# Performance work log

Measured on AMD Instinct MI355X. Metric: run time of the kernel, lower is better.

## Reference

```python
import jax, jax.numpy as jnp
import numpy as np

N = 50000
E = 1600000
D = 128
NUM_CLASSES = 10
SLOPE = 0.01  # torch leaky_relu default


def leaky_relu(x):
    return jnp.where(x >= 0, x, SLOPE * x)


def gcn_conv(x, src, dst, norm_out, norm_in, W, b):
    # DGL GraphConv, norm='both': D_out^{-1/2} A^T D_in^{-1/2} applied as
    # scale-src -> scatter-sum to dst -> scale-dst, then linear + bias.
    h = x * norm_out[:, None]                        # [N, D]
    agg = jax.ops.segment_sum(h[src], dst, num_segments=N)  # [N, D]
    agg = agg * norm_in[:, None]
    return agg @ W + b


def setup_inputs() -> dict:
    key = jax.random.key(0)
    ks = jax.random.split(key, 12)
    def w(k, shape, fan_in):
        return jax.random.normal(k, shape, dtype=jnp.float32) / np.sqrt(fan_in)
    return {
        "x": jax.random.normal(ks[0], (N, D), dtype=jnp.float32),
        "src": jax.random.randint(ks[1], (E,), 0, N),
        "dst": jax.random.randint(ks[2], (E,), 0, N),
        "W1": w(ks[3], (D, D), D),
        "b1": jnp.zeros((D,), jnp.float32),
        "W2": w(ks[4], (D, D), D),
        "b2": jnp.zeros((D,), jnp.float32),
        "agg_w": w(ks[5], (D, 1), D),
        "agg_b": jnp.zeros((1,), jnp.float32),
        "d1_w": w(ks[6], (N, 100), N),
        "d1_b": jnp.zeros((100,), jnp.float32),
        "d2_w": w(ks[7], (100, 20), 100),
        "d2_b": jnp.zeros((20,), jnp.float32),
        "d3_w": w(ks[8], (20, NUM_CLASSES), 20),
        "d3_b": jnp.zeros((NUM_CLASSES,), jnp.float32),
    }


def reference(x, src, dst, W1, b1, W2, b2, agg_w, agg_b,
              d1_w, d1_b, d2_w, d2_b, d3_w, d3_b):
    ones = jnp.ones((E,), jnp.float32)
    out_deg = jax.ops.segment_sum(ones, src, num_segments=N)
    in_deg = jax.ops.segment_sum(ones, dst, num_segments=N)
    # DGL clamps degrees to min 1 (allow_zero_in_degree path)
    norm_out = jnp.power(jnp.clip(out_deg, 1.0), -0.5)
    norm_in = jnp.power(jnp.clip(in_deg, 1.0), -0.5)

    h = gcn_conv(x, src, dst, norm_out, norm_in, W1, b1)
    h = leaky_relu(h)
    h = gcn_conv(h, src, dst, norm_out, norm_in, W2, b2)
    h = h @ agg_w + agg_b            # [N, 1]
    # dropout omitted (eval mode / identity)
    h = h.reshape(-1, N)             # [1, N]
    h = h @ d1_w + d1_b              # [1, 100]
    h = leaky_relu(h @ d2_w + d2_b)  # [1, 20]
    h = h @ d3_w + d3_b              # [1, num_classes]
    return h.reshape(1, -1)
```

## Files before the change

kernel.cpp:

```cpp
#include <hip/hip_runtime.h>
#include <hip/hip_bf16.h>

#define SLOPE 0.01f
#define D 128
#define CAP 64
#define NB 512
#define KE 13
#define SBUF (KE * 256)
#define NPMAX 1024
#define ZB 512
#define ZIT 10

__device__ __forceinline__ float us2f(unsigned int u) {
    union { unsigned int i; float f; } c; c.i = u << 16; return c.f;
}
__device__ __forceinline__ unsigned int f2us(float f) {
    union { float f; unsigned int i; } c; c.f = f;
    return (c.i + 0x7fffu + ((c.i >> 16) & 1u)) >> 16;
}

__global__ void __launch_bounds__(256) k_hist782(const int* __restrict__ dst,
                                                 unsigned int* __restrict__ histg,
                                                 unsigned int* __restrict__ odeg,
                                                 int E, int NP, int N) {
    __shared__ int lb[NPMAX];
    int b = blockIdx.x;
    for (int i = b * 256 + threadIdx.x; i < N; i += NB * 256) odeg[i] = 0u;
    for (int i = threadIdx.x; i < NP; i += 256) lb[i] = 0;
    __syncthreads();
    int ch = (E + NB - 1) / NB;
    int e0 = b * ch, e1 = min(E, e0 + ch);
    for (int e = e0 + threadIdx.x; e < e1; e += 256) atomicAdd(&lb[dst[e] >> 6], 1);
    __syncthreads();
    unsigned int* row = histg + (size_t)b * NP;
    for (int i = threadIdx.x; i < NP; i += 256) row[i] = (unsigned int)lb[i];
}

__global__ void __launch_bounds__(NB) k_scanA(const unsigned int* __restrict__ histg,
                                              unsigned int* __restrict__ boffT,
                                              unsigned int* __restrict__ tot, int NP) {
    __shared__ int wsum[NB / 64];
    int p = blockIdx.x, tid = threadIdx.x, lane = tid & 63, w = tid >> 6;
    int val = (int)histg[(size_t)tid * NP + p];
    int sc = val;
    for (int off = 1; off < 64; off <<= 1) { int t = __shfl_up(sc, off, 64); if (lane >= off) sc += t; }
    if (lane == 63) wsum[w] = sc;
    __syncthreads();
    if (w == 0 && lane < NB / 64) {
        int v4 = wsum[lane];
        for (int off = 1; off < NB / 64; off <<= 1) { int t = __shfl_up(v4, off, 64); if (lane >= off) v4 += t; }
        wsum[lane] = v4;
    }
    __syncthreads();
    int excl = ((w == 0) ? 0 : wsum[w - 1]) + sc - val;
    boffT[(size_t)p * NB + tid] = (unsigned int)excl;
    if (tid == NB - 1) tot[p] = (unsigned int)(excl + val);
}

__global__ void __launch_bounds__(1024) k_misc(const unsigned int* __restrict__ tot,
                                               int* __restrict__ pbase, int NP,
                                               const float* __restrict__ W2, const float* __restrict__ b2,
                                               const float* __restrict__ agg_w, const float* __restrict__ agg_b,
                                               float* __restrict__ v, float* __restrict__ c) {
    __shared__ int wsum[16];
    __shared__ float aw[D];
    __shared__ float red[D];
    int tid = threadIdx.x;
    if (blockIdx.x == 0) {
        int lane = tid & 63, w = tid >> 6;
        int val = (tid < NP) ? (int)tot[tid] : 0;
        int sc = val;
        for (int off = 1; off < 64; off <<= 1) { int t = __shfl_up(sc, off, 64); if (lane >= off) sc += t; }
        if (lane == 63) wsum[w] = sc;
        __syncthreads();
        if (w == 0 && lane < 16) {
            int v16 = wsum[lane];
            for (int off = 1; off < 16; off <<= 1) { int t = __shfl_up(v16, off, 64); if (lane >= off) v16 += t; }
            wsum[lane] = v16;
        }
        __syncthreads();
        int excl = ((w == 0) ? 0 : wsum[w - 1]) + sc - val;
        if (tid <= NP) pbase[tid] = excl;
    } else {
        if (tid >= 128) return;
        aw[tid] = agg_w[tid];
        __syncthreads();
        float acc = 0.f;
        for (int j = 0; j < D; j++) acc += W2[tid * D + j] * aw[j];
        v[tid] = acc;
        red[tid] = b2[tid] * aw[tid];
        __syncthreads();
        for (int off = 64; off > 0; off >>= 1) {
            if (tid < off) red[tid] += red[tid + off];
            __syncthreads();
        }
        if (tid == 0) c[0] = red[0] + agg_b[0];
    }
}

__global__ void __launch_bounds__(256) k_psort(const int* __restrict__ src, const int* __restrict__ dst,
                                               const int* __restrict__ pbase,
                                               const unsigned int* __restrict__ boffT,
                                               unsigned int* __restrict__ parted,
                                               unsigned int* __restrict__ odeg, int E, int NP) {
    __shared__ int lhist[NPMAX];
    __shared__ int lstart[NPMAX];
    __shared__ unsigned int sbuf[SBUF];
    __shared__ int wsum[4];
    int b = blockIdx.x, tid = threadIdx.x, lane = tid & 63, w = tid >> 6;
    for (int i = tid; i < NPMAX; i += 256) lhist[i] = 0;
    __syncthreads();
    int ch = (E + NB - 1) / NB;
    int e0 = b * ch, e1 = min(E, e0 + ch);

    unsigned int rec[KE];
#pragma unroll
    for (int k = 0; k < KE; k++) {
        int e = e0 + k * 256 + tid;
        rec[k] = 0xffffffffu;
        if (e < e1) {
            int d = dst[e], s = src[e];
            atomicAdd(&odeg[s], 1u);
            rec[k] = (unsigned int)s | ((unsigned int)(d & 63) << 16) | ((unsigned int)(d >> 6) << 22);
            atomicAdd(&lhist[d >> 6], 1);
        }
    }
    __syncthreads();

    int base4 = tid * 4;
    int v0 = lhist[base4], v1 = lhist[base4 + 1], v2 = lhist[base4 + 2], v3 = lhist[base4 + 3];
    int tsum = v0 + v1 + v2 + v3;
    int sc = tsum;
    for (int off = 1; off < 64; off <<= 1) { int t = __shfl_up(sc, off, 64); if (lane >= off) sc += t; }
    if (lane == 63) wsum[w] = sc;
    __syncthreads();
    if (w == 0 && lane < 4) {
        int vv = wsum[lane];
        for (int off = 1; off < 4; off <<= 1) { int t = __shfl_up(vv, off, 64); if (lane >= off) vv += t; }
        wsum[lane] = vv;
    }
    __syncthreads();
    int excl = ((w == 0) ? 0 : wsum[w - 1]) + sc - tsum;
    lstart[base4]     = excl;
    lstart[base4 + 1] = excl + v0;
    lstart[base4 + 2] = excl + v0 + v1;
    lstart[base4 + 3] = excl + v0 + v1 + v2;
    __syncthreads();
    for (int i = tid; i < NP; i += 256) {
        int ex = lstart[i];
        lhist[i] = ex;
        lstart[i] = pbase[i] + (int)boffT[(size_t)i * NB + b] - ex;
    }
    __syncthreads();

#pragma unroll
    for (int k = 0; k < KE; k++) {
        if (rec[k] != 0xffffffffu) {
            int p = rec[k] >> 22;
            int pos = atomicAdd(&lhist[p], 1);
            sbuf[pos] = rec[k];
        }
    }
    __syncthreads();

    int totl = e1 - e0;
    for (int j = tid; j < totl; j += 256) {
        unsigned int r = sbuf[j];
        parted[lstart[r >> 22] + j] = r & 0x3fffffu;
    }
}

__global__ void __launch_bounds__(256) k_bfill(
    const int* __restrict__ poff, const unsigned int* __restrict__ parted,
    unsigned short* __restrict__ bucket, int* __restrict__ cnt_in,
    float* __restrict__ norm_in, int N) {
    __shared__ int lcnt[64];
    __shared__ unsigned short blds[64 * CAP];
    int p = blockIdx.x, tid = threadIdx.x;
    if (tid < 64) lcnt[tid] = 0;
    unsigned int sent2 = (unsigned int)N | ((unsigned int)N << 16);
    for (int i = tid; i < 64 * CAP / 2; i += 256) ((unsigned int*)blds)[i] = sent2;
    __syncthreads();
    int e0 = poff[p], e1 = poff[p + 1];
    for (int i = e0 + tid; i < e1; i += 256) {
        unsigned int rec = parted[i];
        int dl = rec >> 16;
        int pos = atomicAdd(&lcnt[dl], 1);
        if (pos < CAP) blds[dl * CAP + pos] = (unsigned short)(rec & 0xffffu);
    }
    __syncthreads();
    int nmax = min(64, N - (p << 6));
    unsigned int* bg = (unsigned int*)(bucket + ((long)p << 6) * CAP);
    const unsigned int* bl = (const unsigned int*)blds;
    for (int i = tid; i < nmax * (CAP / 2); i += 256) bg[i] = bl[i];
    if (tid < nmax) {
        cnt_in[(p << 6) + tid] = lcnt[tid];
        norm_in[(p << 6) + tid] = rsqrtf(fmaxf((float)lcnt[tid], 1.0f));
    }
}

__global__ void k_prep(const float2* __restrict__ x2, const unsigned int* __restrict__ odeg,
                       unsigned int* __restrict__ xb, int N) {
    int g = blockIdx.x * blockDim.x + threadIdx.x;
    int node = g >> 6;
    if (node > N) return;
    int u = g & 63;
    int pass = u >> 4, fu = u & 15;
    unsigned int outv = 0u;
    if (node < N) {
        float no = rsqrtf(fmaxf((float)odeg[node], 1.0f));
        float2 p = x2[g];
        outv = f2us(p.x * no) | (f2us(p.y * no) << 16);
    }
    xb[((size_t)pass * (N + 1) + node) * 16 + fu] = outv;
}

__global__ void __launch_bounds__(256) k_gather1(
    const int* __restrict__ cnt_in, const unsigned short* __restrict__ bucket,
    const unsigned int* __restrict__ xb, unsigned int* __restrict__ agg, int N) {
    int b = blockIdx.x;
    int xcd = b & 7;
    int pass = xcd >> 1;
    int idx = ((b >> 3) << 1) + (xcd & 1);
    int tid = threadIdx.x;
    int node = idx * 4 + (tid >> 6);
    if (node >= N) return;
    int lane = tid & 63;
    int slot = lane >> 4;
    int fu = lane & 15;
    int deg = min(__builtin_nontemporal_load(cnt_in + node), CAP);
    int myedge = (int)__builtin_nontemporal_load(bucket + (long)node * CAP + lane);
    const unsigned int* xq = xb + (size_t)pass * (N + 1) * 16 + fu;
    float ax = 0.f, ay = 0.f;
    {
        unsigned int pv[8];
#pragma unroll
        for (int i = 0; i < 8; i++) {
            int s = __shfl(myedge, i * 4 + slot, 64);
            pv[i] = xq[(size_t)s << 4];
        }
#pragma unroll
        for (int i = 0; i < 8; i++) {
            ax += us2f(pv[i] & 0xffffu);
            ay += us2f(pv[i] >> 16);
        }
    }
    if (deg > 32) {
        unsigned int pv[8];
#pragma unroll
        for (int i = 0; i < 8; i++) {
            int s = __shfl(myedge, 32 + i * 4 + slot, 64);
            pv[i] = xq[(size_t)s << 4];
        }
#pragma unroll
        for (int i = 0; i < 8; i++) {
            ax += us2f(pv[i] & 0xffffu);
            ay += us2f(pv[i] >> 16);
        }
    }
    ax += __shfl_xor(ax, 16, 64); ay += __shfl_xor(ay, 16, 64);
    ax += __shfl_xor(ax, 32, 64); ay += __shfl_xor(ay, 32, 64);
    if (slot == 0)
        __builtin_nontemporal_store(f2us(ax) | (f2us(ay) << 16),
                                    agg + (long)node * 64 + (pass << 4) + fu);
}

__global__ void __launch_bounds__(256) k_lin1q(
    const unsigned int* __restrict__ agg, const float* __restrict__ W1,
    const float* __restrict__ b1, const float* __restrict__ v,
    const unsigned int* __restrict__ odeg, const float* __restrict__ norm_in,
    float* __restrict__ q, int N) {
    __shared__ __align__(16) unsigned int at[64 * 64];
    int tid = threadIdx.x;
    int cg = tid & 31;
    int rg = tid >> 5;
    int r0 = blockIdx.x * 64;

    {
        const uint4* ag4 = (const uint4*)agg;
        uint4* at4 = (uint4*)at;
        uint4 z4; z4.x = z4.y = z4.z = z4.w = 0u;
#pragma unroll
        for (int it = 0; it < 4; it++) {
            int idx = tid + it * 256;
            int r = idx >> 4;
            at4[idx] = (r0 + r < N) ? ag4[(long)(r0 + r) * 16 + (idx & 15)] : z4;
        }
    }
    __syncthreads();

    float4 acc[8];
#pragma unroll
    for (int i = 0; i < 8; i++) acc[i].x = acc[i].y = acc[i].z = acc[i].w = 0.f;

    const float4* W4 = (const float4*)W1;
    const uint4* a4 = ((const uint4*)at) + rg * 8 * 16;
    for (int kq = 0; kq < 16; kq++) {
        float4 w0 = W4[(kq * 8 + 0) * 32 + cg];
        float4 w1 = W4[(kq * 8 + 1) * 32 + cg];
        float4 w2 = W4[(kq * 8 + 2) * 32 + cg];
        float4 w3 = W4[(kq * 8 + 3) * 32 + cg];
        float4 w4 = W4[(kq * 8 + 4) * 32 + cg];
        float4 w5 = W4[(kq * 8 + 5) * 32 + cg];
        float4 w6 = W4[(kq * 8 + 6) * 32 + cg];
        float4 w7 = W4[(kq * 8 + 7) * 32 + cg];
#pragma unroll
        for (int i = 0; i < 8; i++) {
            uint4 a = a4[i * 16 + kq];
            float f0 = us2f(a.x & 0xffffu), f1 = us2f(a.x >> 16);
            float f2 = us2f(a.y & 0xffffu), f3 = us2f(a.y >> 16);
            float f4 = us2f(a.z & 0xffffu), f5 = us2f(a.z >> 16);
            float f6 = us2f(a.w & 0xffffu), f7 = us2f(a.w >> 16);
            acc[i].x += f0*w0.x + f1*w1.x + f2*w2.x + f3*w3.x + f4*w4.x + f5*w5.x + f6*w6.x + f7*w7.x;
            acc[i].y += f0*w0.y + f1*w1.y + f2*w2.y + f3*w3.y + f4*w4.y + f5*w5.y + f6*w6.y + f7*w7.y;
            acc[i].z += f0*w0.z + f1*w1.z + f2*w2.z + f3*w3.z + f4*w4.z + f5*w5.z + f6*w6.z + f7*w7.z;
            acc[i].w += f0*w0.w + f1*w1.w + f2*w2.w + f3*w3.w + f4*w4.w + f5*w5.w + f6*w6.w + f7*w7.w;
        }
    }

    float4 bv = ((const float4*)b1)[cg];
    float4 vv = ((const float4*)v)[cg];
#pragma unroll
    for (int i = 0; i < 8; i++) {
        int row = r0 + rg * 8 + i;
        bool valid = row < N;
        float ni = valid ? norm_in[row] : 0.f;
        float hx = ni * acc[i].x + bv.x; hx = hx >= 0.f ? hx : SLOPE * hx;
        float hy = ni * acc[i].y + bv.y; hy = hy >= 0.f ? hy : SLOPE * hy;
        float hz = ni * acc[i].z + bv.z; hz = hz >= 0.f ? hz : SLOPE * hz;
        float hw = ni * acc[i].w + bv.w; hw = hw >= 0.f ? hw : SLOPE * hw;
        float p = hx * vv.x + hy * vv.y + hz * vv.z + hw * vv.w;
        p += __shfl_down(p, 16, 32);
        p += __shfl_down(p, 8, 32);
        p += __shfl_down(p, 4, 32);
        p += __shfl_down(p, 2, 32);
        p += __shfl_down(p, 1, 32);
        if ((tid & 31) == 0 && valid)
            q[row] = rsqrtf(fmaxf((float)odeg[row], 1.0f)) * p;
    }
}

__global__ void __launch_bounds__(256) k_gather2(
    const int* __restrict__ cnt_in, const unsigned short* __restrict__ bucket,
    const float* __restrict__ q, const float* __restrict__ norm_in,
    const float* __restrict__ c, float* __restrict__ s, int N) {
    int tid = threadIdx.x;
    int node = blockIdx.x * 8 + (tid >> 5);
    int lane = tid & 31;
    if (node >= N) return;
    int deg = min(cnt_in[node], CAP);
    float t = 0.f;
    for (int j = lane; j < deg; j += 32) t += q[(int)bucket[(long)node * CAP + j]];
    t += __shfl_down(t, 16, 32);
    t += __shfl_down(t, 8, 32);
    t += __shfl_down(t, 4, 32);
    t += __shfl_down(t, 2, 32);
    t += __shfl_down(t, 1, 32);
    if (lane == 0) s[node] = norm_in[node] * t + c[0];
}

__global__ void __launch_bounds__(256) k_z1(const float* __restrict__ s,
                                            const float* __restrict__ d1w,
                                            float* __restrict__ zpart, int N) {
    __shared__ float ls[ZIT * 10];
    __shared__ float4 part[256];
    int tid = threadIdx.x;
    int qd = tid % 25;
    int rl = tid / 25;
    int rows_per = (N + gridDim.x - 1) / gridDim.x;
    int r0 = blockIdx.x * rows_per;
    int r1 = min(N, r0 + rows_per);
    if (tid < ZIT * 10) ls[tid] = (r0 + tid < r1) ? s[r0 + tid] : 0.f;
    __syncthreads();
    const float4* w4 = (const float4*)d1w;
    float4 acc; acc.x = acc.y = acc.z = acc.w = 0.f;
    if (tid < 250) {
#pragma unroll
        for (int it = 0; it < ZIT; it++) {
            int ro = rl + it * 10;
            float sv = ls[ro];
            int rr = min(r0 + ro, N - 1);
            float4 w = w4[(long)rr * 25 + qd];
            acc.x += sv * w.x; acc.y += sv * w.y; acc.z += sv * w.z; acc.w += sv * w.w;
        }
    }
    part[tid] = acc;
    __syncthreads();
    if (tid < 25) {
        float4 t = part[tid];
#pragma unroll
        for (int g = 1; g < 10; g++) {
            float4 p = part[tid + 25 * g];
            t.x += p.x; t.y += p.y; t.z += p.z; t.w += p.w;
        }
        ((float4*)zpart)[blockIdx.x * 25 + tid] = t;
    }
}

__global__ void __launch_bounds__(1024) k_tail(const float* __restrict__ zpart,
                                               const float* __restrict__ d1b,
                                               const float* __restrict__ d2w, const float* __restrict__ d2b,
                                               const float* __restrict__ d3w, const float* __restrict__ d3b,
                                               float* __restrict__ out) {
    __shared__ float z1c[100];
    __shared__ float z2c[20];
    int tid = threadIdx.x;
    if (tid < 100) z1c[tid] = 0.f;
    __syncthreads();
    if (tid < 1000) {
        int col = tid % 100;
        int bg = tid / 100;
        float acc = 0.f;
        for (int b = bg; b < ZB; b += 10) acc += zpart[(size_t)b * 100 + col];
        atomicAdd(&z1c[col], acc);
    }
    __syncthreads();
    if (tid < 100) z1c[tid] += d1b[tid];
    __syncthreads();
    if (tid < 20) {
        float acc = d2b[tid];
        for (int k = 0; k < 100; k++) acc += z1c[k] * d2w[k * 20 + tid];
        z2c[tid] = acc >= 0.f ? acc : SLOPE * acc;
    }
    __syncthreads();
    if (tid < 10) {
        float acc = d3b[tid];
        for (int j = 0; j < 20; j++) acc += z2c[j] * d3w[j * 10 + tid];
        out[tid] = acc;
    }
}

extern "C" void kernel_launch(void* const* d_in, const int* in_sizes, int n_in,
                              void* d_out, int out_size, void* d_ws, size_t ws_size,
                              hipStream_t stream) {
    const int N = in_sizes[0] / D;
    const int E = in_sizes[1];
    const int NP = (N + 63) >> 6;

    const float* x     = (const float*)d_in[0];
    const int* src     = (const int*)d_in[1];
    const int* dst     = (const int*)d_in[2];
    const float* W1    = (const float*)d_in[3];
    const float* b1    = (const float*)d_in[4];
    const float* W2    = (const float*)d_in[5];
    const float* b2    = (const float*)d_in[6];
    const float* agg_w = (const float*)d_in[7];
    const float* agg_b = (const float*)d_in[8];
    const float* d1w   = (const float*)d_in[9];
    const float* d1b   = (const float*)d_in[10];
    const float* d2w   = (const float*)d_in[11];
    const float* d2b   = (const float*)d_in[12];
    const float* d3w   = (const float*)d_in[13];
    const float* d3b   = (const float*)d_in[14];
    float* out = (float*)d_out;

    unsigned int* xb  = (unsigned int*)d_ws;
    unsigned int* histg  = xb;
    unsigned int* boffT  = histg + (size_t)NB * NP;
    unsigned int* tot    = boffT + (size_t)NP * NB;
    unsigned int* agg = xb + (size_t)(N + 1) * 64;
    unsigned int* parted = agg;
    unsigned int* odeg   = agg + (size_t)N * 64;
    float* norm_in    = (float*)(odeg + N);
    float* q          = norm_in + N;
    float* s          = q + N;
    float* v          = s + N;
    float* c          = v + 128;
    int* pbase        = (int*)(c + 4);
    int* cnt_in       = pbase + NP + 16;
    unsigned short* bucket = (unsigned short*)(cnt_in + N);
    float* zpart      = (float*)(bucket + (size_t)N * CAP);


    k_hist782<<<NB, 256, 0, stream>>>(dst, histg, odeg, E, NP, N);
    k_scanA<<<NP, NB, 0, stream>>>(histg, boffT, tot, NP);
    k_misc<<<2, 1024, 0, stream>>>(tot, pbase, NP, W2, b2, agg_w, agg_b, v, c);
    k_psort<<<NB, 256, 0, stream>>>(src, dst, pbase, boffT, parted, odeg, E, NP);
    k_bfill<<<NP, 256, 0, stream>>>(pbase, parted, bucket, cnt_in, norm_in, N);
    k_prep<<<((N + 1) * 64 + 255) / 256, 256, 0, stream>>>((const float2*)x, odeg, xb, N);

    {
        const int G = (N + 3) / 4;
        const int G2 = (G + 1) / 2;
        k_gather1<<<8 * G2, 256, 0, stream>>>(cnt_in, bucket, xb, agg, N);
    }
    k_lin1q<<<(N + 63) / 64, 256, 0, stream>>>(agg, W1, b1, v, odeg, norm_in, q, N);
    k_gather2<<<(N + 7) / 8, 256, 0, stream>>>(cnt_in, bucket, q, norm_in, c, s, N);
    k_z1<<<ZB, 256, 0, stream>>>(s, d1w, zpart, N);
    k_tail<<<1, 1024, 0, stream>>>(zpart, d1b, d2w, d2b, d3w, d3b, out);
}
```

Baseline: 354.1 us.

## Replace out-degree global atomics with LDS byte histograms and coarsen dst partitions

Out-degrees are no longer counted with scattered global atomics inside the partition sort. Instead, per-block shared-memory histograms pack four 8-bit counters per word over src, and a separate reduction kernel sums them and writes norm_out directly. The destination partitioning moves from 64-node to 1024-node ranges with more, smaller sort blocks, which shrinks the per-block histogram and scan work. In exchange, each bucket-fill block now scans the whole 1024-node range and filters for its own 64 nodes, so the partitioned edges are read 16 times over. The 8-bit counters also assume fewer than 256 edges per source node in any one block's chunk.

```diff
diff --git a/kernel.cpp b/kernel.cpp
--- a/kernel.cpp
+++ b/kernel.cpp
@@ -4,10 +4,13 @@
 #define SLOPE 0.01f
 #define D 128
 #define CAP 64
-#define NB 512
-#define KE 13
+#define NB 1024
+#define KE 7
 #define SBUF (KE * 256)
-#define NPMAX 1024
+#define NRMAX 64
+#define HBK 256
+#define HBINSB 50176
+#define HWB (HBINSB / 4)
 #define ZB 512
 #define ZIT 10
 
@@ -19,29 +22,62 @@
     return (c.i + 0x7fffu + ((c.i >> 16) & 1u)) >> 16;
 }
 
-__global__ void __launch_bounds__(256) k_hist782(const int* __restrict__ dst,
-                                                 unsigned int* __restrict__ histg,
-                                                 unsigned int* __restrict__ odeg,
-                                                 int E, int NP, int N) {
-    __shared__ int lb[NPMAX];
+__global__ void __launch_bounds__(256) k_hista(const int* __restrict__ src,
+                                               unsigned int* __restrict__ hist,
+                                               int E, int N, int npass) {
+    __shared__ unsigned int lh[HWB];
     int b = blockIdx.x;
-    for (int i = b * 256 + threadIdx.x; i < N; i += NB * 256) odeg[i] = 0u;
-    for (int i = threadIdx.x; i < NP; i += 256) lb[i] = 0;
+    int chunk = (E + gridDim.x - 1) / gridDim.x;
+    int e0 = b * chunk, e1 = min(E, e0 + chunk);
+    int base = 0;
+    for (int p = 0; p < npass; p++, base += HBINSB) {
+        for (int i = threadIdx.x; i < HWB; i += 256) lh[i] = 0;
+        __syncthreads();
+        for (int e = e0 + threadIdx.x; e < e1; e += 256) {
+            unsigned int r = (unsigned int)(src[e] - base);
+            if (r < HBINSB) atomicAdd(&lh[r >> 2], 1u << ((r & 3u) << 3));
+        }
+        __syncthreads();
+        unsigned int* outp = hist + ((size_t)b * npass + p) * HWB;
+        for (int i = threadIdx.x; i < HWB; i += 256) outp[i] = lh[i];
+        __syncthreads();
+    }
+}
+
+__global__ void k_norm(const unsigned int* __restrict__ hist,
+                       float* __restrict__ norm_out, int N, int npass) {
+    int i = blockIdx.x * blockDim.x + threadIdx.x;
+    if (i >= N) return;
+    int p = i / HBINSB;
+    int ib = i - p * HBINSB;
+    int w = ib >> 2, sh = (ib & 3) << 3;
+    unsigned int dsum = 0;
+    for (int b = 0; b < HBK; b++)
+        dsum += (hist[((size_t)b * npass + p) * HWB + w] >> sh) & 0xffu;
+    norm_out[i] = rsqrtf(fmaxf((float)dsum, 1.0f));
+}
+
+__global__ void __launch_bounds__(256) k_histc(const int* __restrict__ dst,
+                                               unsigned int* __restrict__ histg,
+                                               int E, int NR) {
+    __shared__ int lb[NRMAX];
+    int b = blockIdx.x;
+    if (threadIdx.x < NRMAX) lb[threadIdx.x] = 0;
     __syncthreads();
     int ch = (E + NB - 1) / NB;
     int e0 = b * ch, e1 = min(E, e0 + ch);
-    for (int e = e0 + threadIdx.x; e < e1; e += 256) atomicAdd(&lb[dst[e] >> 6], 1);
-    __syncthreads();
-    unsigned int* row = histg + (size_t)b * NP;
-    for (int i = threadIdx.x; i < NP; i += 256) row[i] = (unsigned int)lb[i];
+    for (int e = e0 + threadIdx.x; e < e1; e += 256) atomicAdd(&lb[dst[e] >> 10], 1);
+    __syncthreads();
+    unsigned int* row = histg + (size_t)b * NRMAX;
+    if (threadIdx.x < NRMAX) row[threadIdx.x] = (unsigned int)lb[threadIdx.x];
 }
 
 __global__ void __launch_bounds__(NB) k_scanA(const unsigned int* __restrict__ histg,
                                               unsigned int* __restrict__ boffT,
-                                              unsigned int* __restrict__ tot, int NP) {
+                                              unsigned int* __restrict__ tot, int NR) {
     __shared__ int wsum[NB / 64];
     int p = blockIdx.x, tid = threadIdx.x, lane = tid & 63, w = tid >> 6;
-    int val = (int)histg[(size_t)tid * NP + p];
+    int val = (int)histg[(size_t)tid * NRMAX + p];
     int sc = val;
     for (int off = 1; off < 64; off <<= 1) { int t = __shfl_up(sc, off, 64); if (lane >= off) sc += t; }
     if (lane == 63) wsum[w] = sc;
@@ -58,7 +94,7 @@
 }
 
 __global__ void __launch_bounds__(1024) k_misc(const unsigned int* __restrict__ tot,
-                                               int* __restrict__ pbase, int NP,
+                                               int* __restrict__ rbase, int NR,
                                                const float* __restrict__ W2, const float* __restrict__ b2,
                                                const float* __restrict__ agg_w, const float* __restrict__ agg_b,
                                                float* __restrict__ v, float* __restrict__ c) {
@@ -68,7 +104,7 @@
     int tid = threadIdx.x;
     if (blockIdx.x == 0) {
         int lane = tid & 63, w = tid >> 6;
-        int val = (tid < NP) ? (int)tot[tid] : 0;
+        int val = (tid < NR) ? (int)tot[tid] : 0;
         int sc = val;
         for (int off = 1; off < 64; off <<= 1) { int t = __shfl_up(sc, off, 64); if (lane >= off) sc += t; }
         if (lane == 63) wsum[w] = sc;
@@ -80,7 +116,7 @@
         }
         __syncthreads();
         int excl = ((w == 0) ? 0 : wsum[w - 1]) + sc - val;
-        if (tid <= NP) pbase[tid] = excl;
+        if (tid <= NR) rbase[tid] = excl;
     } else {
         if (tid >= 128) return;
         aw[tid] = agg_w[tid];
@@ -99,16 +135,14 @@
 }
 
 __global__ void __launch_bounds__(256) k_psort(const int* __restrict__ src, const int* __restrict__ dst,
-                                               const int* __restrict__ pbase,
+                                               const int* __restrict__ rbase,
                                                const unsigned int* __restrict__ boffT,
-                                               unsigned int* __restrict__ parted,
-                                               unsigned int* __restrict__ odeg, int E, int NP) {
-    __shared__ int lhist[NPMAX];
-    __shared__ int lstart[NPMAX];
+                                               unsigned int* __restrict__ parted, int E, int NR) {
+    __shared__ int lhist[NRMAX];
+    __shared__ int lstart[NRMAX];
     __shared__ unsigned int sbuf[SBUF];
-    __shared__ int wsum[4];
-    int b = blockIdx.x, tid = threadIdx.x, lane = tid & 63, w = tid >> 6;
-    for (int i = tid; i < NPMAX; i += 256) lhist[i] = 0;
+    int b = blockIdx.x, tid = threadIdx.x;
+    if (tid < NRMAX) lhist[tid] = 0;
     __syncthreads();
     int ch = (E + NB - 1) / NB;
     int e0 = b * ch, e1 = min(E, e0 + ch);
@@ -120,43 +154,26 @@
         rec[k] = 0xffffffffu;
         if (e < e1) {
             int d = dst[e], s = src[e];
-            atomicAdd(&odeg[s], 1u);
-            rec[k] = (unsigned int)s | ((unsigned int)(d & 63) << 16) | ((unsigned int)(d >> 6) << 22);
-            atomicAdd(&lhist[d >> 6], 1);
-        }
-    }
-    __syncthreads();
-
-    int base4 = tid * 4;
-    int v0 = lhist[base4], v1 = lhist[base4 + 1], v2 = lhist[base4 + 2], v3 = lhist[base4 + 3];
-    int tsum = v0 + v1 + v2 + v3;
-    int sc = tsum;
-    for (int off = 1; off < 64; off <<= 1) { int t = __shfl_up(sc, off, 64); if (lane >= off) sc += t; }
-    if (lane == 63) wsum[w] = sc;
-    __syncthreads();
-    if (w == 0 && lane < 4) {
-        int vv = wsum[lane];
-        for (int off = 1; off < 4; off <<= 1) { int t = __shfl_up(vv, off, 64); if (lane >= off) vv += t; }
-        wsum[lane] = vv;
-    }
-    __syncthreads();
-    int excl = ((w == 0) ? 0 : wsum[w - 1]) + sc - tsum;
-    lstart[base4]     = excl;
-    lstart[base4 + 1] = excl + v0;
-    lstart[base4 + 2] = excl + v0 + v1;
-    lstart[base4 + 3] = excl + v0 + v1 + v2;
-    __syncthreads();
-    for (int i = tid; i < NP; i += 256) {
-        int ex = lstart[i];
-        lhist[i] = ex;
-        lstart[i] = pbase[i] + (int)boffT[(size_t)i * NB + b] - ex;
+            rec[k] = (unsigned int)s | ((unsigned int)(d & 1023) << 16) | ((unsigned int)(d >> 10) << 26);
+            atomicAdd(&lhist[d >> 10], 1);
+        }
+    }
+    __syncthreads();
+
+    if (tid < 64) {
+        int val = lhist[tid];
+        int sc = val;
+        for (int off = 1; off < 64; off <<= 1) { int t = __shfl_up(sc, off, 64); if (tid >= off) sc += t; }
+        int ex = sc - val;
+        lhist[tid] = ex;
+        lstart[tid] = (tid < NR) ? (rbase[tid] + (int)boffT[(size_t)tid * NB + b] - ex) : 0;
     }
     __syncthreads();
 
 #pragma unroll
     for (int k = 0; k < KE; k++) {
         if (rec[k] != 0xffffffffu) {
-            int p = rec[k] >> 22;
+            int p = rec[k] >> 26;
             int pos = atomicAdd(&lhist[p], 1);
             sbuf[pos] = rec[k];
         }
@@ -166,27 +183,31 @@
     int totl = e1 - e0;
     for (int j = tid; j < totl; j += 256) {
         unsigned int r = sbuf[j];
-        parted[lstart[r >> 22] + j] = r & 0x3fffffu;
+        parted[lstart[r >> 26] + j] = r & 0x03ffffffu;
     }
 }
 
 __global__ void __launch_bounds__(256) k_bfill(
-    const int* __restrict__ poff, const unsigned int* __restrict__ parted,
+    const int* __restrict__ rbase, const unsigned int* __restrict__ parted,
     unsigned short* __restrict__ bucket, int* __restrict__ cnt_in,
     float* __restrict__ norm_in, int N) {
     __shared__ int lcnt[64];
     __shared__ unsigned short blds[64 * CAP];
     int p = blockIdx.x, tid = threadIdx.x;
+    int r = p >> 4, pr = p & 15;
     if (tid < 64) lcnt[tid] = 0;
     unsigned int sent2 = (unsigned int)N | ((unsigned int)N << 16);
     for (int i = tid; i < 64 * CAP / 2; i += 256) ((unsigned int*)blds)[i] = sent2;
     __syncthreads();
-    int e0 = poff[p], e1 = poff[p + 1];
+    int e0 = rbase[r], e1 = rbase[r + 1];
     for (int i = e0 + tid; i < e1; i += 256) {
         unsigned int rec = parted[i];
-        int dl = rec >> 16;
-        int pos = atomicAdd(&lcnt[dl], 1);
-        if (pos < CAP) blds[dl * CAP + pos] = (unsigned short)(rec & 0xffffu);
+        int nl = (rec >> 16) & 1023;
+        if ((nl >> 6) == pr) {
+            int dl = nl & 63;
+            int pos = atomicAdd(&lcnt[dl], 1);
+            if (pos < CAP) blds[dl * CAP + pos] = (unsigned short)(rec & 0xffffu);
+        }
     }
     __syncthreads();
     int nmax = min(64, N - (p << 6));
@@ -199,7 +220,7 @@
     }
 }
 
-__global__ void k_prep(const float2* __restrict__ x2, const unsigned int* __restrict__ odeg,
+__global__ void k_prep(const float2* __restrict__ x2, const float* __restrict__ norm_out,
                        unsigned int* __restrict__ xb, int N) {
     int g = blockIdx.x * blockDim.x + threadIdx.x;
     int node = g >> 6;
@@ -208,7 +229,7 @@
     int pass = u >> 4, fu = u & 15;
     unsigned int outv = 0u;
     if (node < N) {
-        float no = rsqrtf(fmaxf((float)odeg[node], 1.0f));
+        float no = norm_out[node];
         float2 p = x2[g];
         outv = f2us(p.x * no) | (f2us(p.y * no) << 16);
     }
@@ -268,7 +289,7 @@
 __global__ void __launch_bounds__(256) k_lin1q(
     const unsigned int* __restrict__ agg, const float* __restrict__ W1,
     const float* __restrict__ b1, const float* __restrict__ v,
-    const unsigned int* __restrict__ odeg, const float* __restrict__ norm_in,
+    const float* __restrict__ norm_out, const float* __restrict__ norm_in,
     float* __restrict__ q, int N) {
     __shared__ __align__(16) unsigned int at[64 * 64];
     int tid = threadIdx.x;
@@ -336,7 +357,7 @@
         p += __shfl_down(p, 2, 32);
         p += __shfl_down(p, 1, 32);
         if ((tid & 31) == 0 && valid)
-            q[row] = rsqrtf(fmaxf((float)odeg[row], 1.0f)) * p;
+            q[row] = norm_out[row] * p;
     }
 }
 
@@ -436,6 +457,8 @@
     const int N = in_sizes[0] / D;
     const int E = in_sizes[1];
     const int NP = (N + 63) >> 6;
+    const int NR = (N + 1023) >> 10;
+    const int npass = (N + HBINSB - 1) / HBINSB;
 
     const float* x     = (const float*)d_in[0];
     const int* src     = (const int*)d_in[1];
@@ -456,35 +479,37 @@
 
     unsigned int* xb  = (unsigned int*)d_ws;
     unsigned int* histg  = xb;
-    unsigned int* boffT  = histg + (size_t)NB * NP;
-    unsigned int* tot    = boffT + (size_t)NP * NB;
+    unsigned int* boffT  = histg + (size_t)NB * NRMAX;
+    unsigned int* tot    = boffT + (size_t)NRMAX * NB;
+    unsigned int* histA  = tot + 128;
     unsigned int* agg = xb + (size_t)(N + 1) * 64;
     unsigned int* parted = agg;
-    unsigned int* odeg   = agg + (size_t)N * 64;
-    float* norm_in    = (float*)(odeg + N);
+    float* norm_out   = (float*)(agg + (size_t)N * 64);
+    float* norm_in    = norm_out + N;
     float* q          = norm_in + N;
     float* s          = q + N;
     float* v          = s + N;
     float* c          = v + 128;
-    int* pbase        = (int*)(c + 4);
-    int* cnt_in       = pbase + NP + 16;
+    int* rbase        = (int*)(c + 4);
+    int* cnt_in       = rbase + NRMAX + 16;
     unsigned short* bucket = (unsigned short*)(cnt_in + N);
     float* zpart      = (float*)(bucket + (size_t)N * CAP);
 
-
-    k_hist782<<<NB, 256, 0, stream>>>(dst, histg, odeg, E, NP, N);
-    k_scanA<<<NP, NB, 0, stream>>>(histg, boffT, tot, NP);
-    k_misc<<<2, 1024, 0, stream>>>(tot, pbase, NP, W2, b2, agg_w, agg_b, v, c);
-    k_psort<<<NB, 256, 0, stream>>>(src, dst, pbase, boffT, parted, odeg, E, NP);
-    k_bfill<<<NP, 256, 0, stream>>>(pbase, parted, bucket, cnt_in, norm_in, N);
-    k_prep<<<((N + 1) * 64 + 255) / 256, 256, 0, stream>>>((const float2*)x, odeg, xb, N);
+    k_hista<<<HBK, 256, 0, stream>>>(src, histA, E, N, npass);
+    k_histc<<<NB, 256, 0, stream>>>(dst, histg, E, NR);
+    k_scanA<<<NR, NB, 0, stream>>>(histg, boffT, tot, NR);
+    k_misc<<<2, 1024, 0, stream>>>(tot, rbase, NR, W2, b2, agg_w, agg_b, v, c);
+    k_norm<<<(N + 255) / 256, 256, 0, stream>>>(histA, norm_out, N, npass);
+    k_psort<<<NB, 256, 0, stream>>>(src, dst, rbase, boffT, parted, E, NR);
+    k_bfill<<<NP, 256, 0, stream>>>(rbase, parted, bucket, cnt_in, norm_in, N);
+    k_prep<<<((N + 1) * 64 + 255) / 256, 256, 0, stream>>>((const float2*)x, norm_out, xb, N);
 
     {
         const int G = (N + 3) / 4;
         const int G2 = (G + 1) / 2;
         k_gather1<<<8 * G2, 256, 0, stream>>>(cnt_in, bucket, xb, agg, N);
     }
-    k_lin1q<<<(N + 63) / 64, 256, 0, stream>>>(agg, W1, b1, v, odeg, norm_in, q, N);
+    k_lin1q<<<(N + 63) / 64, 256, 0, stream>>>(agg, W1, b1, v, norm_out, norm_in, q, N);
     k_gather2<<<(N + 7) / 8, 256, 0, stream>>>(cnt_in, bucket, q, norm_in, c, s, N);
     k_z1<<<ZB, 256, 0, stream>>>(s, d1w, zpart, N);
     k_tail<<<1, 1024, 0, stream>>>(zpart, d1b, d2w, d2b, d3w, d3b, out);
```

Measured after the change: 372.9 us. 5.3% more time.
